# Optimization experiments

Hardware: AMD Instinct MI355X
Metric: run time of the kernel (lower is better)

## Reference

```python
import jax, jax.numpy as jnp
import numpy as np

BATCH, IN_F, OUT_F, GRID_PLUS_ORDER = 8192, 1024, 1024, 8

def setup_inputs() -> dict:
    key = jax.random.key(0)
    k1, k2, k3 = jax.random.split(key, 3)
    x = jax.random.normal(k1, (BATCH, IN_F), dtype=jnp.float32)
    base_weight = jax.random.normal(k2, (OUT_F, IN_F), dtype=jnp.float32) * 0.03
    spline_weight = jax.random.normal(k3, (OUT_F, IN_F, GRID_PLUS_ORDER), dtype=jnp.float32) * 0.1
    return {"x": x, "base_weight": base_weight, "spline_weight": spline_weight}

def reference(x, base_weight, spline_weight):
    # base_output = F.linear(x, base_weight) -> x @ W_b^T
    base_output = x @ base_weight.T  # [B, out]
    # Original: sum_{i,g} silu(x)[b,i] * spline_weight[o,i,g]
    # The grid/order axis g is never contracted with x, so it collapses:
    # silu(x) @ spline_weight.sum(-1).T  -- identical math, no [O,B,I,G] blowup.
    w_spline = jnp.sum(spline_weight, axis=-1)  # [out, in]
    spline_output = jax.nn.silu(x) @ w_spline.T  # [B, out]
    return base_output + spline_output
```

## Files before the change

### kernel.cpp

```cpp
#include <hip/hip_runtime.h>
#include <hip/hip_bf16.h>


#define BATCH 8192
#define IN_F 1024
#define OUT_F 1024
#define KP 2048

typedef unsigned short ushort_t;
typedef __attribute__((ext_vector_type(8))) short short8;
typedef __attribute__((ext_vector_type(4))) float f32x4;

__device__ __forceinline__ ushort_t f2bf(float f) {
  union { float f; unsigned int u; } v;
  v.f = f;
  unsigned int u = v.u;
  u += 0x7fffu + ((u >> 16) & 1u);
  return (ushort_t)(u >> 16);
}

__device__ __forceinline__ void async16(const ushort_t* g, ushort_t* l) {
  __builtin_amdgcn_global_load_lds(
      (const __attribute__((address_space(1))) void*)g,
      (__attribute__((address_space(3))) void*)l, 16, 0, 0);
}

#define PREP_A_BLOCKS 4096
#define PREP_S_BLOCKS 1024
#define PREP_B_BLOCKS 1024
#define PREP_BLOCKS (PREP_A_BLOCKS + PREP_S_BLOCKS + PREP_B_BLOCKS)

__global__ __launch_bounds__(256) void prep_all(
    const float* __restrict__ x, const float* __restrict__ Wb,
    const float* __restrict__ Ws, ushort_t* __restrict__ Apack,
    ushort_t* __restrict__ Wpack) {
  const int blk = blockIdx.x;
  const int t = threadIdx.x;

  if (blk < PREP_A_BLOCKS) {
    const int idx = blk * 256 + t;
    const int b = idx >> 7;
    const int i = (idx & 127) << 3;
    const float4 x0 = *(const float4*)(x + ((size_t)b << 10) + i);
    const float4 x1 = *(const float4*)(x + ((size_t)b << 10) + i + 4);
    float xv[8] = {x0.x, x0.y, x0.z, x0.w, x1.x, x1.y, x1.z, x1.w};
    ushort_t vb[8], vs[8];
#pragma unroll
    for (int j = 0; j < 8; ++j) {
      vb[j] = f2bf(xv[j]);
      vs[j] = f2bf(xv[j] / (1.0f + __expf(-xv[j])));
    }
    ushort_t* row = Apack + ((size_t)b << 11);
    *(short8*)(row + i) = *(short8*)vb;
    *(short8*)(row + IN_F + i) = *(short8*)vs;
  } else if (blk < PREP_A_BLOCKS + PREP_S_BLOCKS) {
    const int idx = (blk - PREP_A_BLOCKS) * 256 + t;
    const int o = idx >> 8;
    const int i0 = (idx & 255) << 2;
    ushort_t vs[4];
#pragma unroll
    for (int j = 0; j < 4; ++j) {
      const float4* p = (const float4*)(Ws + ((((size_t)o << 10) + i0 + j) << 3));
      const float4 a = p[0];
      const float4 b = p[1];
      vs[j] = f2bf(((a.x + a.y) + (a.z + a.w)) + ((b.x + b.y) + (b.z + b.w)));
    }
    *(ushort4*)(Wpack + ((size_t)o << 11) + IN_F + i0) = *(ushort4*)vs;
  } else {
    const int idx = (blk - PREP_A_BLOCKS - PREP_S_BLOCKS) * 256 + t;
    const int o = idx >> 8;
    const int c = (idx & 255) << 2;
    const float4 w = *(const float4*)(Wb + ((size_t)o << 10) + c);
    ushort4 v;
    v.x = f2bf(w.x); v.y = f2bf(w.y); v.z = f2bf(w.z); v.w = f2bf(w.w);
    *(ushort4*)(Wpack + ((size_t)o << 11) + c) = v;
  }
}

__global__ __launch_bounds__(256) void gemm_packed(
    const ushort_t* __restrict__ A,
    const ushort_t* __restrict__ W,
    float* __restrict__ C) {
  __shared__ ushort_t As[128 * 32];
  __shared__ ushort_t Bs[128 * 32];

  const int t = threadIdx.x;
  const int flat = blockIdx.y * 8 + blockIdx.x;
  const int xcd = flat & 7;
  const int local = flat >> 3;
  const int nt = local >> 3;
  const int mt = xcd * 8 + (local & 7);

  const int lane = t & 63;
  const int wave = t >> 6;
  const int wr = wave >> 1;
  const int wc = wave & 1;

  const int srow = t >> 2;
  const int scol = (t & 3) << 3;
  const size_t a_g0 = ((size_t)(mt * 128 + srow)) * KP + scol;
  const size_t b_g0 = ((size_t)(nt * 128 + srow)) * KP + scol;
  ushort_t* as_d = As + t * 8;
  ushort_t* bs_d = Bs + t * 8;

  f32x4 acc[4][4];
#pragma unroll
  for (int mi = 0; mi < 4; ++mi)
#pragma unroll
    for (int ni = 0; ni < 4; ++ni) acc[mi][ni] = (f32x4){0.f, 0.f, 0.f, 0.f};

  const int arow = wr * 64 + (lane & 15);
  const int brow = wc * 64 + (lane & 15);
  const int kofs = (lane >> 4) << 3;

  for (int k0 = 0; k0 < KP; k0 += 32) {
    __syncthreads();
    async16(A + a_g0 + k0, as_d);
    async16(A + a_g0 + k0 + (size_t)64 * KP, as_d + 2048);
    async16(W + b_g0 + k0, bs_d);
    async16(W + b_g0 + k0 + (size_t)64 * KP, bs_d + 2048);
    __syncthreads();

    short8 af[4], bfr[4];
#pragma unroll
    for (int mi = 0; mi < 4; ++mi)
      af[mi] = *(const short8*)(As + (arow + mi * 16) * 32 + kofs);
#pragma unroll
    for (int ni = 0; ni < 4; ++ni)
      bfr[ni] = *(const short8*)(Bs + (brow + ni * 16) * 32 + kofs);

#pragma unroll
    for (int mi = 0; mi < 4; ++mi)
#pragma unroll
      for (int ni = 0; ni < 4; ++ni)
        acc[mi][ni] = __builtin_amdgcn_mfma_f32_16x16x32_bf16(af[mi], bfr[ni], acc[mi][ni], 0, 0, 0);
  }

  const int col0 = nt * 128 + wc * 64 + (lane & 15);
  const int row0 = mt * 128 + wr * 64 + ((lane >> 4) << 2);
#pragma unroll
  for (int mi = 0; mi < 4; ++mi)
#pragma unroll
    for (int ni = 0; ni < 4; ++ni) {
      float* cp = C + (size_t)(row0 + mi * 16) * OUT_F + col0 + ni * 16;
#pragma unroll
      for (int r = 0; r < 4; ++r) cp[(size_t)r * OUT_F] = acc[mi][ni][r];
    }
}

extern "C" void kernel_launch(void* const* d_in, const int* in_sizes, int n_in,
                              void* d_out, int out_size, void* d_ws, size_t ws_size,
                              hipStream_t stream) {
  const float* x = (const float*)d_in[0];
  const float* wb = (const float*)d_in[1];
  const float* ws = (const float*)d_in[2];
  float* out = (float*)d_out;

  ushort_t* Apack = (ushort_t*)d_ws;
  ushort_t* Wpack = (ushort_t*)((char*)d_ws + (size_t)BATCH * KP * 2);

  prep_all<<<PREP_BLOCKS, 256, 0, stream>>>(x, wb, ws, Apack, Wpack);
  gemm_packed<<<dim3(OUT_F / 128, BATCH / 128), 256, 0, stream>>>(Apack, Wpack, out);
}
```

Baseline: 161.7 us.

## Double-buffer LDS tiles and use k-slot-major layout in bf16 GEMM

The GEMM now keeps two LDS buffers per operand. It prefetches the next 32-wide K tile with global_load_lds while MFMAs run on the current one, and drops one of the two barriers per iteration. The shared tile layout changes from row-major [128][32] to k-slot-major [4][128][8], so each 16-lane group reads contiguous 16-byte rows, which should cut LDS bank conflicts. The cost is twice the LDS footprint, which may reduce occupancy. Correctness also depends on the barrier waiting for the async LDS loads to finish.

```diff
diff --git a/kernel.cpp b/kernel.cpp
--- a/kernel.cpp
+++ b/kernel.cpp
@@ -81,8 +81,8 @@
     const ushort_t* __restrict__ A,
     const ushort_t* __restrict__ W,
     float* __restrict__ C) {
-  __shared__ ushort_t As[128 * 32];
-  __shared__ ushort_t Bs[128 * 32];
+  __shared__ ushort_t As[2 * 4096];
+  __shared__ ushort_t Bs[2 * 4096];
 
   const int t = threadIdx.x;
   const int flat = blockIdx.y * 8 + blockIdx.x;
@@ -96,12 +96,11 @@
   const int wr = wave >> 1;
   const int wc = wave & 1;
 
-  const int srow = t >> 2;
-  const int scol = (t & 3) << 3;
-  const size_t a_g0 = ((size_t)(mt * 128 + srow)) * KP + scol;
-  const size_t b_g0 = ((size_t)(nt * 128 + srow)) * KP + scol;
-  ushort_t* as_d = As + t * 8;
-  ushort_t* bs_d = Bs + t * 8;
+  const int srow = t & 127;
+  const int sslot = t >> 7;
+  const ushort_t* a_g = A + ((size_t)(mt * 128 + srow)) * KP + sslot * 8;
+  const ushort_t* b_g = W + ((size_t)(nt * 128 + srow)) * KP + sslot * 8;
+  const int t8 = t * 8;
 
   f32x4 acc[4][4];
 #pragma unroll
@@ -111,23 +110,33 @@
 
   const int arow = wr * 64 + (lane & 15);
   const int brow = wc * 64 + (lane & 15);
-  const int kofs = (lane >> 4) << 3;
+  const int rk = (lane >> 4) * 1024;
 
-  for (int k0 = 0; k0 < KP; k0 += 32) {
+  async16(a_g, As + t8);
+  async16(a_g + 16, As + 2048 + t8);
+  async16(b_g, Bs + t8);
+  async16(b_g + 16, Bs + 2048 + t8);
+
+  int p = 0;
+  for (int k0 = 0; k0 < KP; k0 += 32, p ^= 1) {
     __syncthreads();
-    async16(A + a_g0 + k0, as_d);
-    async16(A + a_g0 + k0 + (size_t)64 * KP, as_d + 2048);
-    async16(W + b_g0 + k0, bs_d);
-    async16(W + b_g0 + k0 + (size_t)64 * KP, bs_d + 2048);
-    __syncthreads();
+    if (k0 + 32 < KP) {
+      const int q = p ^ 1;
+      async16(a_g + k0 + 32, As + q * 4096 + t8);
+      async16(a_g + k0 + 48, As + q * 4096 + 2048 + t8);
+      async16(b_g + k0 + 32, Bs + q * 4096 + t8);
+      async16(b_g + k0 + 48, Bs + q * 4096 + 2048 + t8);
+    }
 
+    const ushort_t* ab = As + p * 4096 + rk;
+    const ushort_t* bb = Bs + p * 4096 + rk;
     short8 af[4], bfr[4];
 #pragma unroll
     for (int mi = 0; mi < 4; ++mi)
-      af[mi] = *(const short8*)(As + (arow + mi * 16) * 32 + kofs);
+      af[mi] = *(const short8*)(ab + (arow + mi * 16) * 8);
 #pragma unroll
     for (int ni = 0; ni < 4; ++ni)
-      bfr[ni] = *(const short8*)(Bs + (brow + ni * 16) * 32 + kofs);
+      bfr[ni] = *(const short8*)(bb + (brow + ni * 16) * 8);
 
 #pragma unroll
     for (int mi = 0; mi < 4; ++mi)
```

Measured after the change: 190.0 us. 17.5% more time.

## Double-buffer GEMM LDS tiles with register prefetch and XOR-swizzled layout

Applied to the files above, without the earlier changes.

Replaces the synchronous global_load_lds staging with a register-prefetch, double-buffered LDS pipeline. The next K tile is loaded into registers while the current tile's MFMAs run, then written to the alternate buffer, so there is one barrier per iteration instead of two. The LDS layout becomes k-slice-major with an XOR row swizzle to cut bank conflicts on the fragment reads. The cost is twice the LDS, extra VGPRs for the prefetched data, and VALU LDS writes in place of the async copy path.

```diff
diff --git a/kernel.cpp b/kernel.cpp
--- a/kernel.cpp
+++ b/kernel.cpp
@@ -17,12 +17,6 @@
   unsigned int u = v.u;
   u += 0x7fffu + ((u >> 16) & 1u);
   return (ushort_t)(u >> 16);
-}
-
-__device__ __forceinline__ void async16(const ushort_t* g, ushort_t* l) {
-  __builtin_amdgcn_global_load_lds(
-      (const __attribute__((address_space(1))) void*)g,
-      (__attribute__((address_space(3))) void*)l, 16, 0, 0);
 }
 
 #define PREP_A_BLOCKS 4096
@@ -81,8 +75,8 @@
     const ushort_t* __restrict__ A,
     const ushort_t* __restrict__ W,
     float* __restrict__ C) {
-  __shared__ ushort_t As[128 * 32];
-  __shared__ ushort_t Bs[128 * 32];
+  __shared__ ushort_t As[2 * 4096];
+  __shared__ ushort_t Bs[2 * 4096];
 
   const int t = threadIdx.x;
   const int flat = blockIdx.y * 8 + blockIdx.x;
@@ -96,12 +90,12 @@
   const int wr = wave >> 1;
   const int wc = wave & 1;
 
-  const int srow = t >> 2;
-  const int scol = (t & 3) << 3;
-  const size_t a_g0 = ((size_t)(mt * 128 + srow)) * KP + scol;
-  const size_t b_g0 = ((size_t)(nt * 128 + srow)) * KP + scol;
-  ushort_t* as_d = As + t * 8;
-  ushort_t* bs_d = Bs + t * 8;
+  const int r = t >> 2;
+  const int c = t & 3;
+  const ushort_t* a_g = A + ((size_t)(mt * 128 + r)) * KP + c * 8;
+  const ushort_t* b_g = W + ((size_t)(nt * 128 + r)) * KP + c * 8;
+  const size_t rowskip = (size_t)64 * KP;
+  const int wbase = c * 1024 + ((r ^ (c << 2)) << 3);
 
   f32x4 acc[4][4];
 #pragma unroll
@@ -109,31 +103,59 @@
 #pragma unroll
     for (int ni = 0; ni < 4; ++ni) acc[mi][ni] = (f32x4){0.f, 0.f, 0.f, 0.f};
 
-  const int arow = wr * 64 + (lane & 15);
-  const int brow = wc * 64 + (lane & 15);
-  const int kofs = (lane >> 4) << 3;
+  const int ks = lane >> 4;
+  const int ar = (wr * 64 + (lane & 15)) ^ (ks << 2);
+  const int br = (wc * 64 + (lane & 15)) ^ (ks << 2);
+  const int rbase = ks * 1024;
 
+  {
+    uint4 la0 = *(const uint4*)(a_g);
+    uint4 la1 = *(const uint4*)(a_g + rowskip);
+    uint4 lb0 = *(const uint4*)(b_g);
+    uint4 lb1 = *(const uint4*)(b_g + rowskip);
+    *(uint4*)(As + wbase) = la0;
+    *(uint4*)(As + wbase + 512) = la1;
+    *(uint4*)(Bs + wbase) = lb0;
+    *(uint4*)(Bs + wbase + 512) = lb1;
+  }
+  __syncthreads();
+
+  int poff = 0;
   for (int k0 = 0; k0 < KP; k0 += 32) {
-    __syncthreads();
-    async16(A + a_g0 + k0, as_d);
-    async16(A + a_g0 + k0 + (size_t)64 * KP, as_d + 2048);
-    async16(W + b_g0 + k0, bs_d);
-    async16(W + b_g0 + k0 + (size_t)64 * KP, bs_d + 2048);
-    __syncthreads();
+    const bool more = (k0 + 32) < KP;
+    uint4 na0, na1, nb0, nb1;
+    if (more) {
+      na0 = *(const uint4*)(a_g + k0 + 32);
+      na1 = *(const uint4*)(a_g + k0 + 32 + rowskip);
+      nb0 = *(const uint4*)(b_g + k0 + 32);
+      nb1 = *(const uint4*)(b_g + k0 + 32 + rowskip);
+    }
 
+    const ushort_t* ab = As + poff + rbase;
+    const ushort_t* bb = Bs + poff + rbase;
     short8 af[4], bfr[4];
 #pragma unroll
     for (int mi = 0; mi < 4; ++mi)
-      af[mi] = *(const short8*)(As + (arow + mi * 16) * 32 + kofs);
+      af[mi] = *(const short8*)(ab + ((ar + mi * 16) << 3));
 #pragma unroll
     for (int ni = 0; ni < 4; ++ni)
-      bfr[ni] = *(const short8*)(Bs + (brow + ni * 16) * 32 + kofs);
+      bfr[ni] = *(const short8*)(bb + ((br + ni * 16) << 3));
 
 #pragma unroll
     for (int mi = 0; mi < 4; ++mi)
 #pragma unroll
       for (int ni = 0; ni < 4; ++ni)
         acc[mi][ni] = __builtin_amdgcn_mfma_f32_16x16x32_bf16(af[mi], bfr[ni], acc[mi][ni], 0, 0, 0);
+
+    if (more) {
+      const int qoff = poff ^ 4096;
+      *(uint4*)(As + qoff + wbase) = na0;
+      *(uint4*)(As + qoff + wbase + 512) = na1;
+      *(uint4*)(Bs + qoff + wbase) = nb0;
+      *(uint4*)(Bs + qoff + wbase + 512) = nb1;
+      __syncthreads();
+    }
+    poff ^= 4096;
   }
 
   const int col0 = nt * 128 + wc * 64 + (lane & 15);
@@ -144,7 +166,7 @@
     for (int ni = 0; ni < 4; ++ni) {
       float* cp = C + (size_t)(row0 + mi * 16) * OUT_F + col0 + ni * 16;
 #pragma unroll
-      for (int r = 0; r < 4; ++r) cp[(size_t)r * OUT_F] = acc[mi][ni][r];
+      for (int rr = 0; rr < 4; ++rr) cp[(size_t)rr * OUT_F] = acc[mi][ni][rr];
     }
 }
 
```

New measurement: 154.6 us. 1.05x faster.

## Fuse activation bf16/silu conversion into GEMM with register-staged double buffering

Applied to the files above, without the earlier changes.

Removes the separate pass that packed x and silu(x) into a bf16 workspace; the GEMM now loads fp32 x directly, converts (and applies silu for the second K half) in registers, and writes into LDS. LDS is double-buffered with a padded k-slab layout so global loads for the next tile overlap MFMA work on the current one, with one barrier per iteration. This avoids writing and re-reading a 32MB packed activation buffer but recomputes silu/conversion once per N-tile (8x redundant) and reads fp32 x at twice the bytes per K step.

```diff
diff --git a/kernel.cpp b/kernel.cpp
--- a/kernel.cpp
+++ b/kernel.cpp
@@ -6,6 +6,8 @@
 #define IN_F 1024
 #define OUT_F 1024
 #define KP 2048
+#define SLOT 1040
+#define BUF (4 * SLOT)
 
 typedef unsigned short ushort_t;
 typedef __attribute__((ext_vector_type(8))) short short8;
@@ -19,42 +21,25 @@
   return (ushort_t)(u >> 16);
 }
 
-__device__ __forceinline__ void async16(const ushort_t* g, ushort_t* l) {
-  __builtin_amdgcn_global_load_lds(
-      (const __attribute__((address_space(1))) void*)g,
-      (__attribute__((address_space(3))) void*)l, 16, 0, 0);
+__device__ __forceinline__ ushort4 cvt4(float4 v, bool do_silu) {
+  if (do_silu) {
+    v.x = v.x / (1.0f + __expf(-v.x));
+    v.y = v.y / (1.0f + __expf(-v.y));
+    v.z = v.z / (1.0f + __expf(-v.z));
+    v.w = v.w / (1.0f + __expf(-v.w));
+  }
+  ushort4 r;
+  r.x = f2bf(v.x); r.y = f2bf(v.y); r.z = f2bf(v.z); r.w = f2bf(v.w);
+  return r;
 }
 
-#define PREP_A_BLOCKS 4096
-#define PREP_S_BLOCKS 1024
-#define PREP_B_BLOCKS 1024
-#define PREP_BLOCKS (PREP_A_BLOCKS + PREP_S_BLOCKS + PREP_B_BLOCKS)
-
-__global__ __launch_bounds__(256) void prep_all(
-    const float* __restrict__ x, const float* __restrict__ Wb,
-    const float* __restrict__ Ws, ushort_t* __restrict__ Apack,
+__global__ __launch_bounds__(256) void prep_w(
+    const float* __restrict__ Wb, const float* __restrict__ Ws,
     ushort_t* __restrict__ Wpack) {
   const int blk = blockIdx.x;
   const int t = threadIdx.x;
-
-  if (blk < PREP_A_BLOCKS) {
+  if (blk < 1024) {
     const int idx = blk * 256 + t;
-    const int b = idx >> 7;
-    const int i = (idx & 127) << 3;
-    const float4 x0 = *(const float4*)(x + ((size_t)b << 10) + i);
-    const float4 x1 = *(const float4*)(x + ((size_t)b << 10) + i + 4);
-    float xv[8] = {x0.x, x0.y, x0.z, x0.w, x1.x, x1.y, x1.z, x1.w};
-    ushort_t vb[8], vs[8];
-#pragma unroll
-    for (int j = 0; j < 8; ++j) {
-      vb[j] = f2bf(xv[j]);
-      vs[j] = f2bf(xv[j] / (1.0f + __expf(-xv[j])));
-    }
-    ushort_t* row = Apack + ((size_t)b << 11);
-    *(short8*)(row + i) = *(short8*)vb;
-    *(short8*)(row + IN_F + i) = *(short8*)vs;
-  } else if (blk < PREP_A_BLOCKS + PREP_S_BLOCKS) {
-    const int idx = (blk - PREP_A_BLOCKS) * 256 + t;
     const int o = idx >> 8;
     const int i0 = (idx & 255) << 2;
     ushort_t vs[4];
@@ -67,7 +52,7 @@
     }
     *(ushort4*)(Wpack + ((size_t)o << 11) + IN_F + i0) = *(ushort4*)vs;
   } else {
-    const int idx = (blk - PREP_A_BLOCKS - PREP_S_BLOCKS) * 256 + t;
+    const int idx = (blk - 1024) * 256 + t;
     const int o = idx >> 8;
     const int c = (idx & 255) << 2;
     const float4 w = *(const float4*)(Wb + ((size_t)o << 10) + c);
@@ -77,12 +62,12 @@
   }
 }
 
-__global__ __launch_bounds__(256) void gemm_packed(
-    const ushort_t* __restrict__ A,
+__global__ __launch_bounds__(256) void gemm_fused(
+    const float* __restrict__ x,
     const ushort_t* __restrict__ W,
     float* __restrict__ C) {
-  __shared__ ushort_t As[128 * 32];
-  __shared__ ushort_t Bs[128 * 32];
+  __shared__ ushort_t As[2 * BUF];
+  __shared__ ushort_t Bs[2 * BUF];
 
   const int t = threadIdx.x;
   const int flat = blockIdx.y * 8 + blockIdx.x;
@@ -96,12 +81,15 @@
   const int wr = wave >> 1;
   const int wc = wave & 1;
 
-  const int srow = t >> 2;
-  const int scol = (t & 3) << 3;
-  const size_t a_g0 = ((size_t)(mt * 128 + srow)) * KP + scol;
-  const size_t b_g0 = ((size_t)(nt * 128 + srow)) * KP + scol;
-  ushort_t* as_d = As + t * 8;
-  ushort_t* bs_d = Bs + t * 8;
+  const int ar0 = t >> 3;
+  const int aq = t & 7;
+  const float* a_gp = x + ((size_t)(mt * 128 + ar0)) * IN_F + aq * 4;
+  const int a_elem0 = (aq >> 1) * SLOT + (ar0 << 3) + (aq & 1) * 4;
+
+  const int br0 = t >> 2;
+  const int bks = t & 3;
+  const ushort_t* b_gp = W + ((size_t)(nt * 128 + br0)) * KP + bks * 8;
+  const int b_elem0 = bks * SLOT + (br0 << 3);
 
   f32x4 acc[4][4];
 #pragma unroll
@@ -109,31 +97,67 @@
 #pragma unroll
     for (int ni = 0; ni < 4; ++ni) acc[mi][ni] = (f32x4){0.f, 0.f, 0.f, 0.f};
 
+  const int ks1040 = (lane >> 4) * SLOT;
   const int arow = wr * 64 + (lane & 15);
   const int brow = wc * 64 + (lane & 15);
-  const int kofs = (lane >> 4) << 3;
 
+  {
+    float4 fa[4];
+    short8 fb0, fb1;
+#pragma unroll
+    for (int j = 0; j < 4; ++j) fa[j] = *(const float4*)(a_gp + j * 32 * IN_F);
+    fb0 = *(const short8*)(b_gp);
+    fb1 = *(const short8*)(b_gp + (size_t)64 * KP);
+#pragma unroll
+    for (int j = 0; j < 4; ++j)
+      *(ushort4*)(As + a_elem0 + j * 256) = cvt4(fa[j], false);
+    *(short8*)(Bs + b_elem0) = fb0;
+    *(short8*)(Bs + b_elem0 + 512) = fb1;
+  }
+  __syncthreads();
+
+  int poff = 0;
   for (int k0 = 0; k0 < KP; k0 += 32) {
-    __syncthreads();
-    async16(A + a_g0 + k0, as_d);
-    async16(A + a_g0 + k0 + (size_t)64 * KP, as_d + 2048);
-    async16(W + b_g0 + k0, bs_d);
-    async16(W + b_g0 + k0 + (size_t)64 * KP, bs_d + 2048);
-    __syncthreads();
+    const bool more = (k0 + 32) < KP;
+    const int kn = k0 + 32;
+    const int kx = kn & 1023;
+    const bool silu_n = kn >= IN_F;
 
+    float4 fa[4];
+    short8 fb0, fb1;
+    if (more) {
+#pragma unroll
+      for (int j = 0; j < 4; ++j) fa[j] = *(const float4*)(a_gp + kx + j * 32 * IN_F);
+      fb0 = *(const short8*)(b_gp + kn);
+      fb1 = *(const short8*)(b_gp + kn + (size_t)64 * KP);
+    }
+
+    const ushort_t* ab = As + poff + ks1040;
+    const ushort_t* bb = Bs + poff + ks1040;
     short8 af[4], bfr[4];
 #pragma unroll
     for (int mi = 0; mi < 4; ++mi)
-      af[mi] = *(const short8*)(As + (arow + mi * 16) * 32 + kofs);
+      af[mi] = *(const short8*)(ab + ((arow + mi * 16) << 3));
 #pragma unroll
     for (int ni = 0; ni < 4; ++ni)
-      bfr[ni] = *(const short8*)(Bs + (brow + ni * 16) * 32 + kofs);
+      bfr[ni] = *(const short8*)(bb + ((brow + ni * 16) << 3));
 
 #pragma unroll
     for (int mi = 0; mi < 4; ++mi)
 #pragma unroll
       for (int ni = 0; ni < 4; ++ni)
         acc[mi][ni] = __builtin_amdgcn_mfma_f32_16x16x32_bf16(af[mi], bfr[ni], acc[mi][ni], 0, 0, 0);
+
+    if (more) {
+      const int qoff = poff ^ BUF;
+#pragma unroll
+      for (int j = 0; j < 4; ++j)
+        *(ushort4*)(As + qoff + a_elem0 + j * 256) = cvt4(fa[j], silu_n);
+      *(short8*)(Bs + qoff + b_elem0) = fb0;
+      *(short8*)(Bs + qoff + b_elem0 + 512) = fb1;
+      __syncthreads();
+    }
+    poff ^= BUF;
   }
 
   const int col0 = nt * 128 + wc * 64 + (lane & 15);
@@ -144,7 +168,7 @@
     for (int ni = 0; ni < 4; ++ni) {
       float* cp = C + (size_t)(row0 + mi * 16) * OUT_F + col0 + ni * 16;
 #pragma unroll
-      for (int r = 0; r < 4; ++r) cp[(size_t)r * OUT_F] = acc[mi][ni][r];
+      for (int rr = 0; rr < 4; ++rr) cp[(size_t)rr * OUT_F] = acc[mi][ni][rr];
     }
 }
 
@@ -156,9 +180,8 @@
   const float* ws = (const float*)d_in[2];
   float* out = (float*)d_out;
 
-  ushort_t* Apack = (ushort_t*)d_ws;
-  ushort_t* Wpack = (ushort_t*)((char*)d_ws + (size_t)BATCH * KP * 2);
+  ushort_t* Wpack = (ushort_t*)d_ws;
 
-  prep_all<<<PREP_BLOCKS, 256, 0, stream>>>(x, wb, ws, Apack, Wpack);
-  gemm_packed<<<dim3(OUT_F / 128, BATCH / 128), 256, 0, stream>>>(Apack, Wpack, out);
+  prep_w<<<2048, 256, 0, stream>>>(wb, ws, Wpack);
+  gemm_fused<<<dim3(OUT_F / 128, BATCH / 128), 256, 0, stream>>>(x, Wpack, out);
 }
```

After: 220.1 us. +36.1%, slower.
